# Optimization experiments

Hardware: AMD Instinct MI355X
Metric: run time of the kernel (lower is better)

Reference implementation:

```python
import jax, jax.numpy as jnp
import numpy as np

B, E, DIM, RANK, K, P, H, W, FREQ = 16, 4, 64, 32, 2, 8, 128, 128, 64
NOISE_STD = 1.0 / E


def conv1x1(x, w):
    # x: [b,c,h,w], w: [o,c]
    return jnp.einsum('bchw,oc->bohw', x, w)


def dwconv(x, w, pad):
    # depthwise conv, w: [c,1,kh,kw]
    c = x.shape[1]
    return jax.lax.conv_general_dilated(
        x, w, (1, 1), [(pad, pad), (pad, pad)],
        dimension_numbers=('NCHW', 'OIHW', 'NCHW'), feature_group_count=c)


def patchify(x):
    b, c, h, w = x.shape
    return x.reshape(b, c, h // P, P, w // P, P).transpose(0, 1, 2, 4, 3, 5)


def unpatchify(x):
    b, c, hb, wb, p1, p2 = x.shape
    return x.transpose(0, 1, 2, 4, 3, 5).reshape(b, c, hb * p1, wb * p2)


def chan_layernorm(x, w, b):
    # WithBias LayerNorm over channel dim (to_3d puts c last)
    mu = x.mean(axis=1, keepdims=True)
    var = ((x - mu) ** 2).mean(axis=1, keepdims=True)
    return (x - mu) / jnp.sqrt(var + 1e-5) * w[None, :, None, None] + b[None, :, None, None]


def fft_attention(x, qw, qdw, kvw, kvdw, lnw, lnb, pow_, pob):
    q = dwconv(conv1x1(x, qw), qdw, 1)
    kv = dwconv(conv1x1(x, kvw), kvdw, 3)
    k, v = jnp.split(kv, 2, axis=1)
    qf = jnp.fft.rfft2(patchify(q))
    kf = jnp.fft.rfft2(patchify(k))
    out = jnp.fft.irfft2(qf * kf, s=(P, P))
    out = unpatchify(out)
    out = chan_layernorm(out, lnw, lnb)
    out = out * v
    return conv1x1(out, pow_) + pob[None, :, None, None]


def expert(p0, p1, p2, qw, qdw, kvw, kvdw, lnw, lnb, pow_, pob, x, shared):
    # ModExpert.process (feat_extract with depth>1 recomputes the same value)
    xr = conv1x1(x, p0)
    att = fft_attention(xr, qw, qdw, kvw, kvdw, lnw, lnb, pow_, pob)
    g = jax.nn.silu(conv1x1(shared, p1))
    return conv1x1(att * g, p2) + x


def setup_inputs() -> dict:
    key = jax.random.key(0)
    ks = jax.random.split(key, 20)
    s = 0.05
    return {
        'x': jax.random.normal(ks[0], (B, DIM, H, W), jnp.float32),
        'shared': jax.random.normal(ks[1], (B, DIM, H, W), jnp.float32),
        'freq_emb': jax.random.normal(ks[2], (B, FREQ), jnp.float32),
        'noise': jax.random.normal(ks[3], (B, E), jnp.float32),
        'gate_w': jax.random.normal(ks[4], (E, DIM), jnp.float32) * s,
        'freq_gate_w': jax.random.normal(ks[5], (E, FREQ), jnp.float32) * s,
        'p0': jax.random.normal(ks[6], (E, RANK, DIM), jnp.float32) * s,
        'p1': jax.random.normal(ks[7], (E, RANK, DIM), jnp.float32) * s,
        'p2': jax.random.normal(ks[8], (E, DIM, RANK), jnp.float32) * s,
        'q_w': jax.random.normal(ks[9], (E, RANK, RANK), jnp.float32) * s,
        'q_dw': jax.random.normal(ks[10], (E, RANK, 1, 3, 3), jnp.float32) * s,
        'kv_w': jax.random.normal(ks[11], (E, 2 * RANK, RANK), jnp.float32) * s,
        'kv_dw': jax.random.normal(ks[12], (E, 2 * RANK, 1, 7, 7), jnp.float32) * s,
        'ln_w': jnp.ones((E, RANK), jnp.float32),
        'ln_b': jnp.zeros((E, RANK), jnp.float32),
        'po_w': jax.random.normal(ks[13], (E, RANK, RANK), jnp.float32) * s,
        'po_b': jnp.zeros((E, RANK), jnp.float32),
    }


def reference(x, shared, freq_emb, noise, gate_w, freq_gate_w, p0, p1, p2,
              q_w, q_dw, kv_w, kv_dw, ln_w, ln_b, po_w, po_b):
    # RoutingFunction (eval mode: aux_loss = 0, noise still added)
    pooled = x.mean(axis=(2, 3))                       # [B, DIM]
    logits = pooled @ gate_w.T + freq_emb @ freq_gate_w.T  # [B, E]
    noisy = logits + noise * NOISE_STD
    scores = jax.nn.softmax(noisy, axis=-1)
    vals, idx = jax.lax.top_k(scores, K)
    gates = jnp.zeros_like(scores).at[jnp.arange(B)[:, None], idx].set(vals)
    # Dense expert evaluation; gated combine == SparseDispatcher dispatch/combine
    outs = jax.vmap(expert, in_axes=(0,) * 11 + (None, None))(
        p0, p1, p2, q_w, q_dw, kv_w, kv_dw, ln_w, ln_b, po_w, po_b, x, shared)
    return jnp.einsum('be,ebchw->bchw', gates, outs)
```

## Files before the change

### kernel.cpp

```cpp
#include <hip/hip_runtime.h>
#include <hip/hip_bf16.h>

#define BATCH 16
#define DIM 64
#define RANK 32
#define H 128
#define W 128
#define HW (H*W)
#define NSLOT 32

typedef __attribute__((ext_vector_type(8))) short short8;
typedef __attribute__((ext_vector_type(4))) float f32x4;

static __device__ __forceinline__ float bu2f(unsigned short u) {
    return __uint_as_float(((unsigned)u) << 16);
}
static __device__ __forceinline__ unsigned short f2bu(float f) {
    union { __hip_bfloat16 h; unsigned short u; } cv;
    cv.h = __float2bfloat16(f);
    return cv.u;
}
static __device__ __forceinline__ float ulo(unsigned int w) { return __uint_as_float(w << 16); }
static __device__ __forceinline__ float uhi(unsigned int w) { return __uint_as_float(w & 0xffff0000u); }

__global__ __launch_bounds__(256) void k_pool(const float* __restrict__ x,
                                              float* __restrict__ pooled) {
    int bc = blockIdx.x;
    const float4* p = (const float4*)(x + (size_t)bc * HW);
    float s = 0.f;
    for (int i = threadIdx.x; i < HW / 4; i += 256) {
        float4 v = p[i];
        s += v.x + v.y + v.z + v.w;
    }
#pragma unroll
    for (int off = 32; off > 0; off >>= 1) s += __shfl_down(s, off);
    __shared__ float red[4];
    if ((threadIdx.x & 63) == 0) red[threadIdx.x >> 6] = s;
    __syncthreads();
    if (threadIdx.x == 0)
        pooled[bc] = (red[0] + red[1] + red[2] + red[3]) * (1.f / HW);
}

__global__ __launch_bounds__(64) void k_gate(const float* __restrict__ pooled,
                                             const float* __restrict__ freq_emb,
                                             const float* __restrict__ noise,
                                             const float* __restrict__ gate_w,
                                             const float* __restrict__ fgw,
                                             int* __restrict__ slot_e,
                                             float* __restrict__ slot_g,
                                             float* __restrict__ gsum) {
    int b = threadIdx.x;
    if (b >= BATCH) return;
    float lg[4];
    for (int e = 0; e < 4; e++) {
        float s = 0.f;
        for (int c = 0; c < 64; c++) s += pooled[b * 64 + c] * gate_w[e * 64 + c];
        for (int c = 0; c < 64; c++) s += freq_emb[b * 64 + c] * fgw[e * 64 + c];
        s += noise[b * 4 + e] * 0.25f;
        lg[e] = s;
    }
    float m = fmaxf(fmaxf(lg[0], lg[1]), fmaxf(lg[2], lg[3]));
    float sc[4], Z = 0.f;
    for (int e = 0; e < 4; e++) { sc[e] = expf(lg[e] - m); Z += sc[e]; }
    for (int e = 0; e < 4; e++) sc[e] /= Z;
    int i0 = 0;
    for (int e = 1; e < 4; e++) if (sc[e] > sc[i0]) i0 = e;
    int i1 = -1;
    for (int e = 0; e < 4; e++) {
        if (e == i0) continue;
        if (i1 < 0 || sc[e] > sc[i1]) i1 = e;
    }
    slot_e[2 * b] = i0;     slot_g[2 * b] = sc[i0];
    slot_e[2 * b + 1] = i1; slot_g[2 * b + 1] = sc[i1];
    gsum[b] = sc[i0] + sc[i1];
}

__global__ __launch_bounds__(256) void k_weff(const float* __restrict__ q_w,
                                              const float* __restrict__ kv_w,
                                              const float* __restrict__ p0,
                                              unsigned short* __restrict__ weff_h,
                                              unsigned short* __restrict__ weff_l) {
    int t = blockIdx.x * 256 + threadIdx.x;
    if (t >= 4 * 96 * 64) return;
    int c = t & 63;
    int j = (t >> 6) % 96;
    int e = t / (96 * 64);
    const float* p0p = p0 + (size_t)e * RANK * DIM;
    float s = 0.f;
    if (j < 32) {
        const float* qp = q_w + (e * 32 + j) * 32;
        for (int r = 0; r < 32; r++) s += qp[r] * p0p[r * DIM + c];
    } else {
        const float* kp = kv_w + (e * 64 + (j - 32)) * 32;
        for (int r = 0; r < 32; r++) s += kp[r] * p0p[r * DIM + c];
    }
    int idx = (e * 96 + j) * 64 + c;
    unsigned short hv = f2bu(s);
    weff_h[idx] = hv;
    weff_l[idx] = f2bu(s - bu2f(hv));
}

__global__ __launch_bounds__(256) void k_xpose(const float* __restrict__ po_w,
                                               const float* __restrict__ p1,
                                               float* __restrict__ powf,
                                               float* __restrict__ p1f) {
    int t = blockIdx.x * 256 + threadIdx.x;
    if (t < 4096) {
        int e = t >> 10, oc = (t >> 5) & 31, c = t & 31;
        powf[(e * 32 + c) * 32 + oc] = po_w[t];
    }
    int e = t >> 11, j = (t >> 6) & 31, c = t & 63;
    p1f[(e * 64 + c) * 32 + j] = p1[t];
}

__global__ __launch_bounds__(256) void k_qkvpre(const float* __restrict__ x,
                                                const unsigned short* __restrict__ weff_h,
                                                const unsigned short* __restrict__ weff_l,
                                                const int* __restrict__ slot_e,
                                                unsigned short* __restrict__ qkvpre) {
    __shared__ __align__(16) unsigned short XT[2][128 * 64];
    int blk = blockIdx.x;
    int slot = blk >> 7;
    int p0 = (blk & 127) << 7;
    int b = slot >> 1;
    int e = slot_e[slot];

    {
        int t = threadIdx.x;
        int px = t & 127;
        int ch = (t >> 7) << 5;
        const float* xb = x + ((size_t)b * 64 + ch) * HW + p0 + px;
        unsigned short hv[32] __attribute__((aligned(16)));
        unsigned short lv[32] __attribute__((aligned(16)));
#pragma unroll
        for (int c = 0; c < 32; c++) {
            float v = xb[(size_t)c * HW];
            unsigned short h = f2bu(v);
            hv[c] = h;
            lv[c] = f2bu(v - bu2f(h));
        }
        int rowbyte = px * 128;
        int sw = (px & 7) << 4;
#pragma unroll
        for (int k = 0; k < 4; k++) {
            int byt = (rowbyte + (ch + k * 8) * 2) ^ sw;
            *(uint4*)((char*)XT[0] + byt) = *(const uint4*)&hv[k * 8];
            *(uint4*)((char*)XT[1] + byt) = *(const uint4*)&lv[k * 8];
        }
    }
    __syncthreads();

    int w = threadIdx.x >> 6;
    int l = threadIdx.x & 63;
    int li = l & 15, lq = l >> 4;

    short8 Bf[2][2][2];
#pragma unroll
    for (int nt = 0; nt < 2; nt++) {
        int pxl = (w << 5) + (nt << 4) + li;
        int sw = (pxl & 7) << 4;
#pragma unroll
        for (int kt = 0; kt < 2; kt++) {
            int byt = (pxl * 128 + kt * 64 + lq * 16) ^ sw;
            Bf[nt][kt][0] = *(const short8*)((char*)XT[0] + byt);
            Bf[nt][kt][1] = *(const short8*)((char*)XT[1] + byt);
        }
    }

    const unsigned short* wh = weff_h + ((size_t)e * 96 + li) * 64 + lq * 8;
    const unsigned short* wl = weff_l + ((size_t)e * 96 + li) * 64 + lq * 8;

#pragma unroll
    for (int mt = 0; mt < 6; mt++) {
        short8 Ah[2], Al[2];
#pragma unroll
        for (int kt = 0; kt < 2; kt++) {
            Ah[kt] = *(const short8*)(wh + (mt * 16) * 64 + kt * 32);
            Al[kt] = *(const short8*)(wl + (mt * 16) * 64 + kt * 32);
        }
        f32x4 acc[2] = {{0.f, 0.f, 0.f, 0.f}, {0.f, 0.f, 0.f, 0.f}};
#pragma unroll
        for (int nt = 0; nt < 2; nt++) {
#pragma unroll
            for (int kt = 0; kt < 2; kt++) {
                acc[nt] = __builtin_amdgcn_mfma_f32_16x16x32_bf16(Ah[kt], Bf[nt][kt][0], acc[nt], 0, 0, 0);
                acc[nt] = __builtin_amdgcn_mfma_f32_16x16x32_bf16(Ah[kt], Bf[nt][kt][1], acc[nt], 0, 0, 0);
                acc[nt] = __builtin_amdgcn_mfma_f32_16x16x32_bf16(Al[kt], Bf[nt][kt][0], acc[nt], 0, 0, 0);
            }
        }
#pragma unroll
        for (int nt = 0; nt < 2; nt++) {
            int p = p0 + (w << 5) + (nt << 4) + li;
            unsigned short* op = qkvpre + ((size_t)slot * 96 + mt * 16 + lq * 4) * HW + p;
#pragma unroll
            for (int r = 0; r < 4; r++)
                op[(size_t)r * HW] = f2bu(acc[nt][r]);
        }
    }
}

__global__ __launch_bounds__(256) void k_dw(const unsigned short* __restrict__ qkvpre,
                                            const float* __restrict__ q_dw,
                                            const float* __restrict__ kv_dw,
                                            const int* __restrict__ slot_e,
                                            unsigned short* __restrict__ qkv) {
    __shared__ unsigned short S[38][144];
    int t = blockIdx.x;
    int tile = t & 3;
    int c = (t >> 2) % 96;
    int slot = t / (96 * 4);
    int e = slot_e[slot];
    const unsigned short* in = qkvpre + ((size_t)slot * 96 + c) * HW;
    int y0 = tile * 32 - 3;

    float wk[49];
    if (c < 32) {
        const float* wp = q_dw + (e * 32 + c) * 9;
#pragma unroll
        for (int i = 0; i < 9; i++) wk[i] = wp[i];
    } else {
        const float* wp = kv_dw + (e * 64 + (c - 32)) * 49;
#pragma unroll
        for (int i = 0; i < 49; i++) wk[i] = wp[i];
    }

    for (int i = threadIdx.x; i < 38 * 16; i += 256) {
        int r = i >> 4;
        int xc = (i & 15) << 3;
        int yy = y0 + r;
        uint4 v = make_uint4(0u, 0u, 0u, 0u);
        if (yy >= 0 && yy < H) v = *(const uint4*)(in + (size_t)yy * W + xc);
        *(uint4*)&S[r][8 + xc] = v;
    }
    for (int i = threadIdx.x; i < 38 * 2; i += 256) {
        int r = i >> 1;
        *(uint4*)&S[r][(i & 1) ? 136 : 0] = make_uint4(0u, 0u, 0u, 0u);
    }
    __syncthreads();

    int tx = (threadIdx.x & 31) * 4;
    int ty0 = (threadIdx.x >> 5) * 4;
    float acc[4][4];
#pragma unroll
    for (int a_ = 0; a_ < 4; a_++)
#pragma unroll
        for (int b_ = 0; b_ < 4; b_++) acc[a_][b_] = 0.f;

    if (c < 32) {
#pragma unroll
        for (int rr = 0; rr < 6; rr++) {
            int srow = ty0 + 2 + rr;
            float px[12];
            uint2 w0 = *(const uint2*)&S[srow][4 + tx];
            uint2 w1 = *(const uint2*)&S[srow][8 + tx];
            uint2 w2 = *(const uint2*)&S[srow][12 + tx];
            px[0] = ulo(w0.x); px[1] = uhi(w0.x); px[2] = ulo(w0.y); px[3] = uhi(w0.y);
            px[4] = ulo(w1.x); px[5] = uhi(w1.x); px[6] = ulo(w1.y); px[7] = uhi(w1.y);
            px[8] = ulo(w2.x); px[9] = uhi(w2.x); px[10] = ulo(w2.y); px[11] = uhi(w2.y);
#pragma unroll
            for (int ly = 0; ly < 4; ly++) {
                int ky = rr - ly;
                if (ky < 0 || ky > 2) continue;
#pragma unroll
                for (int kx = 0; kx < 3; kx++) {
                    float wv = wk[ky * 3 + kx];
#pragma unroll
                    for (int j = 0; j < 4; j++) acc[ly][j] += wv * px[j + kx + 3];
                }
            }
        }
    } else {
#pragma unroll
        for (int rr = 0; rr < 10; rr++) {
            int srow = ty0 + rr;
            float px[12];
            uint2 w0 = *(const uint2*)&S[srow][4 + tx];
            uint2 w1 = *(const uint2*)&S[srow][8 + tx];
            uint2 w2 = *(const uint2*)&S[srow][12 + tx];
            px[0] = ulo(w0.x); px[1] = uhi(w0.x); px[2] = ulo(w0.y); px[3] = uhi(w0.y);
            px[4] = ulo(w1.x); px[5] = uhi(w1.x); px[6] = ulo(w1.y); px[7] = uhi(w1.y);
            px[8] = ulo(w2.x); px[9] = uhi(w2.x); px[10] = ulo(w2.y); px[11] = uhi(w2.y);
#pragma unroll
            for (int ly = 0; ly < 4; ly++) {
                int ky = rr - ly;
                if (ky < 0 || ky > 6) continue;
#pragma unroll
                for (int kx = 0; kx < 7; kx++) {
                    float wv = wk[ky * 7 + kx];
#pragma unroll
                    for (int j = 0; j < 4; j++) acc[ly][j] += wv * px[j + kx + 1];
                }
            }
        }
    }

    unsigned short* op = qkv + ((size_t)slot * 96 + c) * HW;
    int ybase = tile * 32 + ty0;
#pragma unroll
    for (int ly = 0; ly < 4; ly++) {
        ushort4 o4;
        o4.x = f2bu(acc[ly][0]); o4.y = f2bu(acc[ly][1]);
        o4.z = f2bu(acc[ly][2]); o4.w = f2bu(acc[ly][3]);
        *(ushort4*)(op + (size_t)(ybase + ly) * W + tx) = o4;
    }
}

__global__ __launch_bounds__(256) void k_circ(const unsigned short* __restrict__ qkv,
                                              unsigned short* __restrict__ obuf) {
    __shared__ float Qs[32][68];
    __shared__ float Kp[32][68];
    int u = threadIdx.x >> 3;
    int i = threadIdx.x & 7;
    int U = blockIdx.x * 32 + u;
    int patch = U & 255;
    int c = (U >> 8) & 31;
    int slot = U >> 13;
    int py = patch >> 4, px = patch & 15;
    size_t rowbase = ((size_t)slot * 96 + c) * HW + (py * 8 + i) * W + px * 8;
    uint4 qu = *(const uint4*)(qkv + rowbase);
    uint4 ku = *(const uint4*)(qkv + rowbase + (size_t)32 * HW);
    float qr[8], kr[8];
    qr[0] = ulo(qu.x); qr[1] = uhi(qu.x); qr[2] = ulo(qu.y); qr[3] = uhi(qu.y);
    qr[4] = ulo(qu.z); qr[5] = uhi(qu.z); qr[6] = ulo(qu.w); qr[7] = uhi(qu.w);
    kr[0] = ulo(ku.x); kr[1] = uhi(ku.x); kr[2] = ulo(ku.y); kr[3] = uhi(ku.y);
    kr[4] = ulo(ku.z); kr[5] = uhi(ku.z); kr[6] = ulo(ku.w); kr[7] = uhi(ku.w);
    *(float4*)&Qs[u][i * 8] = *(float4*)&qr[0];
    *(float4*)&Qs[u][i * 8 + 4] = *(float4*)&qr[4];
    *(float4*)&Kp[u][i * 8] = *(float4*)&kr[0];
    *(float4*)&Kp[u][i * 8 + 4] = *(float4*)&kr[4];
    __syncthreads();
    float acc[8];
#pragma unroll
    for (int j = 0; j < 8; j++) acc[j] = 0.f;
#pragma unroll
    for (int mi = 0; mi < 8; mi++) {
        int r = (i - mi) & 7;
        float qv[8], ka[4], kb[4];
        *(float4*)&qv[0] = *(const float4*)&Qs[u][mi * 8];
        *(float4*)&qv[4] = *(const float4*)&Qs[u][mi * 8 + 4];
        *(float4*)&ka[0] = *(const float4*)&Kp[u][r * 8];
        *(float4*)&kb[0] = *(const float4*)&Kp[u][r * 8 + 4];
#pragma unroll
        for (int j = 0; j < 8; j++) {
            float s = acc[j];
#pragma unroll
            for (int t = 0; t < 4; t++) {
                s += ka[t] * qv[(j - t) & 7];
                s += kb[t] * qv[(j - 4 - t) & 7];
            }
            acc[j] = s;
        }
    }
    size_t obase = ((size_t)slot * 32 + c) * HW + (py * 8 + i) * W + px * 8;
    uint4 ov;
    ov.x = (unsigned)f2bu(acc[0]) | ((unsigned)f2bu(acc[1]) << 16);
    ov.y = (unsigned)f2bu(acc[2]) | ((unsigned)f2bu(acc[3]) << 16);
    ov.z = (unsigned)f2bu(acc[4]) | ((unsigned)f2bu(acc[5]) << 16);
    ov.w = (unsigned)f2bu(acc[6]) | ((unsigned)f2bu(acc[7]) << 16);
    *(uint4*)(obuf + obase) = ov;
}

__global__ __launch_bounds__(256) void k_att(const unsigned short* __restrict__ obuf,
                                             const unsigned short* __restrict__ qkv,
                                             const float* __restrict__ shr,
                                             const int* __restrict__ slot_e,
                                             const float* __restrict__ slot_g,
                                             const float* __restrict__ powf,
                                             const float* __restrict__ po_b,
                                             const float* __restrict__ ln_w,
                                             const float* __restrict__ ln_b,
                                             const float* __restrict__ p1f,
                                             unsigned short* __restrict__ attg) {
    int slot = blockIdx.x >> 6;
    int p = ((blockIdx.x & 63) << 8) + threadIdx.x;
    int b = slot >> 1;
    int e = slot_e[slot];
    float g = slot_g[slot];

    const unsigned short* op = obuf + (size_t)slot * 32 * HW + p;
    float o[32];
#pragma unroll
    for (int c = 0; c < 32; c++) o[c] = bu2f(op[(size_t)c * HW]);
    float mu = 0.f;
#pragma unroll
    for (int c = 0; c < 32; c++) mu += o[c];
    mu *= (1.f / 32.f);
    float var = 0.f;
#pragma unroll
    for (int c = 0; c < 32; c++) { float d = o[c] - mu; var += d * d; }
    float rinv = rsqrtf(var * (1.f / 32.f) + 1e-5f);
    const float* powp = powf + e * 1024;
    const float* lnwp = ln_w + e * 32;
    const float* lnbp = ln_b + e * 32;
    const float* pobp = po_b + e * 32;
    const unsigned short* vp = qkv + ((size_t)slot * 96 + 64) * HW + p;
    float att[32];
#pragma unroll
    for (int j = 0; j < 32; j++) att[j] = pobp[j];
    for (int c = 0; c < 32; c++) {
        float uu = ((o[c] - mu) * rinv * lnwp[c] + lnbp[c]) * bu2f(vp[(size_t)c * HW]);
        const float* pr = powp + c * 32;
#pragma unroll
        for (int j = 0; j < 32; j++) att[j] += pr[j] * uu;
    }

    float t[32];
#pragma unroll
    for (int j = 0; j < 32; j++) t[j] = 0.f;
    const float* shp = shr + (size_t)b * 64 * HW + p;
    const float* p1p = p1f + e * 2048;
    for (int c = 0; c < 64; c++) {
        float sv = shp[(size_t)c * HW];
        const float* pr = p1p + c * 32;
#pragma unroll
        for (int j = 0; j < 32; j++) t[j] += pr[j] * sv;
    }

    unsigned short* ap = attg + ((size_t)slot * HW + p) * 32;
    unsigned int wbuf[16];
#pragma unroll
    for (int jj = 0; jj < 16; jj++) {
        float t0 = t[2 * jj], t1 = t[2 * jj + 1];
        float a0 = g * att[2 * jj] * t0 * __builtin_amdgcn_rcpf(1.f + __expf(-t0));
        float a1 = g * att[2 * jj + 1] * t1 * __builtin_amdgcn_rcpf(1.f + __expf(-t1));
        wbuf[jj] = (unsigned)f2bu(a0) | ((unsigned)f2bu(a1) << 16);
    }
#pragma unroll
    for (int q = 0; q < 4; q++)
        *(uint4*)(ap + q * 8) = *(uint4*)&wbuf[q * 4];
}

__global__ __launch_bounds__(256) void k_comb(const unsigned short* __restrict__ attg,
                                              const float* __restrict__ x,
                                              const int* __restrict__ slot_e,
                                              const float* __restrict__ gsum,
                                              const float* __restrict__ p2,
                                              float* __restrict__ out) {
    int t = blockIdx.x;
    int oh = t & 1;
    int tile = (t >> 1) & 63;
    int b = t >> 7;
    int p = (tile << 8) + threadIdx.x;

    const unsigned short* a0p = attg + ((size_t)(2 * b) * HW + p) * 32;
    const unsigned short* a1p = attg + ((size_t)(2 * b + 1) * HW + p) * 32;
    float a0[32], a1[32];
#pragma unroll
    for (int q = 0; q < 4; q++) {
        uint4 u0 = *(const uint4*)(a0p + q * 8);
        uint4 u1 = *(const uint4*)(a1p + q * 8);
        a0[q * 8 + 0] = ulo(u0.x); a0[q * 8 + 1] = uhi(u0.x);
        a0[q * 8 + 2] = ulo(u0.y); a0[q * 8 + 3] = uhi(u0.y);
        a0[q * 8 + 4] = ulo(u0.z); a0[q * 8 + 5] = uhi(u0.z);
        a0[q * 8 + 6] = ulo(u0.w); a0[q * 8 + 7] = uhi(u0.w);
        a1[q * 8 + 0] = ulo(u1.x); a1[q * 8 + 1] = uhi(u1.x);
        a1[q * 8 + 2] = ulo(u1.y); a1[q * 8 + 3] = uhi(u1.y);
        a1[q * 8 + 4] = ulo(u1.z); a1[q * 8 + 5] = uhi(u1.z);
        a1[q * 8 + 6] = ulo(u1.w); a1[q * 8 + 7] = uhi(u1.w);
    }
    int e0 = slot_e[2 * b], e1 = slot_e[2 * b + 1];
    float gs = gsum[b];
    const float* p2a = p2 + e0 * 2048 + oh * 1024;
    const float* p2b = p2 + e1 * 2048 + oh * 1024;
    const float* xp = x + ((size_t)b * 64 + oh * 32) * HW + p;
    float* oa = out + ((size_t)b * 64 + oh * 32) * HW + p;
    for (int oc = 0; oc < 32; oc++) {
        const float* pa = p2a + oc * 32;
        const float* pb = p2b + oc * 32;
        float sa = 0.f, sb = 0.f;
#pragma unroll
        for (int j = 0; j < 32; j++) {
            sa += pa[j] * a0[j];
            sb += pb[j] * a1[j];
        }
        oa[(size_t)oc * HW] = sa + sb + gs * xp[(size_t)oc * HW];
    }
}

extern "C" void kernel_launch(void* const* d_in, const int* in_sizes, int n_in,
                              void* d_out, int out_size, void* d_ws, size_t ws_size,
                              hipStream_t stream) {
    (void)in_sizes; (void)n_in; (void)out_size; (void)ws_size;
    const float* x      = (const float*)d_in[0];
    const float* shr    = (const float*)d_in[1];
    const float* femb   = (const float*)d_in[2];
    const float* noise  = (const float*)d_in[3];
    const float* gate_w = (const float*)d_in[4];
    const float* fgw    = (const float*)d_in[5];
    const float* p0     = (const float*)d_in[6];
    const float* p1     = (const float*)d_in[7];
    const float* p2     = (const float*)d_in[8];
    const float* q_w    = (const float*)d_in[9];
    const float* q_dw   = (const float*)d_in[10];
    const float* kv_w   = (const float*)d_in[11];
    const float* kv_dw  = (const float*)d_in[12];
    const float* ln_w   = (const float*)d_in[13];
    const float* ln_b   = (const float*)d_in[14];
    const float* po_w   = (const float*)d_in[15];
    const float* po_b   = (const float*)d_in[16];
    float* out = (float*)d_out;

    float* fws = (float*)d_ws;
    float* pooled = fws; fws += 1024;
    float* gsum   = fws; fws += 16;
    float* slot_g = fws; fws += 32;
    int*   slot_e = (int*)fws; fws += 32;
    unsigned short* weffh = (unsigned short*)fws; fws += 12288;
    unsigned short* weffl = (unsigned short*)fws; fws += 12288;
    float* powf   = fws; fws += 4096;
    float* p1f    = fws; fws += 8192;
    uintptr_t a = ((uintptr_t)fws + 255) & ~(uintptr_t)255;
    unsigned short* qkvpre = (unsigned short*)a;
    unsigned short* qkvb   = qkvpre + (size_t)NSLOT * 96 * HW;
    unsigned short* obuf   = qkvb + (size_t)NSLOT * 96 * HW;
    unsigned short* attg   = qkvpre;

    k_pool<<<1024, 256, 0, stream>>>(x, pooled);
    k_gate<<<1, 64, 0, stream>>>(pooled, femb, noise, gate_w, fgw, slot_e, slot_g, gsum);
    k_weff<<<96, 256, 0, stream>>>(q_w, kv_w, p0, weffh, weffl);
    k_xpose<<<32, 256, 0, stream>>>(po_w, p1, powf, p1f);
    k_qkvpre<<<NSLOT * 128, 256, 0, stream>>>(x, weffh, weffl, slot_e, qkvpre);
    k_dw<<<NSLOT * 96 * 4, 256, 0, stream>>>(qkvpre, q_dw, kv_dw, slot_e, qkvb);
    k_circ<<<NSLOT * 32 * 256 / 32, 256, 0, stream>>>(qkvb, obuf);
    k_att<<<NSLOT * 64, 256, 0, stream>>>(obuf, qkvb, shr, slot_e, slot_g,
                                          powf, po_b, ln_w, ln_b, p1f, attg);
    k_comb<<<BATCH * 128, 256, 0, stream>>>(attg, x, slot_e, gsum, p2, out);
}
```

Before: 469.1 us.

## Move attention projection and gate matmuls in k_att onto bf16 MFMA with split precision

k_att used per-thread scalar FMA loops for the 32x32 output projection and the 64->32 gate projection. It now stages the normalized, v-scaled activations and the shared features into LDS as hi/lo bf16 pairs in a swizzled layout. It then computes both projections with 16x16x32 bf16 MFMA instructions, using three products (hi*hi, hi*lo, lo*hi) to keep near-fp32 accuracy. The weight preprocessing kernel now emits hi/lo bf16 copies of po_w and p1 instead of transposed fp32, and the grid doubles to 128 pixels per block. The cost is extra LDS use and conversion work, and half the threads sit idle during each staging branch.

Result: faster. 454.2 us (-3.2%).

```diff
diff --git a/kernel.cpp b/kernel.cpp
--- a/kernel.cpp
+++ b/kernel.cpp
@@ -102,15 +102,21 @@
 
 __global__ __launch_bounds__(256) void k_xpose(const float* __restrict__ po_w,
                                                const float* __restrict__ p1,
-                                               float* __restrict__ powf,
-                                               float* __restrict__ p1f) {
+                                               unsigned short* __restrict__ pow_h,
+                                               unsigned short* __restrict__ pow_l,
+                                               unsigned short* __restrict__ p1_h,
+                                               unsigned short* __restrict__ p1_l) {
     int t = blockIdx.x * 256 + threadIdx.x;
     if (t < 4096) {
-        int e = t >> 10, oc = (t >> 5) & 31, c = t & 31;
-        powf[(e * 32 + c) * 32 + oc] = po_w[t];
-    }
-    int e = t >> 11, j = (t >> 6) & 31, c = t & 63;
-    p1f[(e * 64 + c) * 32 + j] = p1[t];
+        float v = po_w[t];
+        unsigned short h = f2bu(v);
+        pow_h[t] = h;
+        pow_l[t] = f2bu(v - bu2f(h));
+    }
+    float v = p1[t];
+    unsigned short h = f2bu(v);
+    p1_h[t] = h;
+    p1_l[t] = f2bu(v - bu2f(h));
 }
 
 __global__ __launch_bounds__(256) void k_qkvpre(const float* __restrict__ x,
@@ -365,69 +371,155 @@
                                              const float* __restrict__ shr,
                                              const int* __restrict__ slot_e,
                                              const float* __restrict__ slot_g,
-                                             const float* __restrict__ powf,
+                                             const unsigned short* __restrict__ pow_h,
+                                             const unsigned short* __restrict__ pow_l,
                                              const float* __restrict__ po_b,
                                              const float* __restrict__ ln_w,
                                              const float* __restrict__ ln_b,
-                                             const float* __restrict__ p1f,
+                                             const unsigned short* __restrict__ p1_h,
+                                             const unsigned short* __restrict__ p1_l,
                                              unsigned short* __restrict__ attg) {
-    int slot = blockIdx.x >> 6;
-    int p = ((blockIdx.x & 63) << 8) + threadIdx.x;
+    __shared__ __align__(16) unsigned short US[128 * 64];
+    __shared__ __align__(16) unsigned short SS[128 * 128];
+    int blk = blockIdx.x;
+    int slot = blk >> 7;
+    int p0 = (blk & 127) << 7;
     int b = slot >> 1;
     int e = slot_e[slot];
     float g = slot_g[slot];
 
-    const unsigned short* op = obuf + (size_t)slot * 32 * HW + p;
-    float o[32];
-#pragma unroll
-    for (int c = 0; c < 32; c++) o[c] = bu2f(op[(size_t)c * HW]);
-    float mu = 0.f;
-#pragma unroll
-    for (int c = 0; c < 32; c++) mu += o[c];
-    mu *= (1.f / 32.f);
-    float var = 0.f;
-#pragma unroll
-    for (int c = 0; c < 32; c++) { float d = o[c] - mu; var += d * d; }
-    float rinv = rsqrtf(var * (1.f / 32.f) + 1e-5f);
-    const float* powp = powf + e * 1024;
-    const float* lnwp = ln_w + e * 32;
-    const float* lnbp = ln_b + e * 32;
-    const float* pobp = po_b + e * 32;
-    const unsigned short* vp = qkv + ((size_t)slot * 96 + 64) * HW + p;
-    float att[32];
-#pragma unroll
-    for (int j = 0; j < 32; j++) att[j] = pobp[j];
-    for (int c = 0; c < 32; c++) {
-        float uu = ((o[c] - mu) * rinv * lnwp[c] + lnbp[c]) * bu2f(vp[(size_t)c * HW]);
-        const float* pr = powp + c * 32;
-#pragma unroll
-        for (int j = 0; j < 32; j++) att[j] += pr[j] * uu;
-    }
-
-    float t[32];
-#pragma unroll
-    for (int j = 0; j < 32; j++) t[j] = 0.f;
-    const float* shp = shr + (size_t)b * 64 * HW + p;
-    const float* p1p = p1f + e * 2048;
-    for (int c = 0; c < 64; c++) {
-        float sv = shp[(size_t)c * HW];
-        const float* pr = p1p + c * 32;
-#pragma unroll
-        for (int j = 0; j < 32; j++) t[j] += pr[j] * sv;
-    }
-
-    unsigned short* ap = attg + ((size_t)slot * HW + p) * 32;
-    unsigned int wbuf[16];
-#pragma unroll
-    for (int jj = 0; jj < 16; jj++) {
-        float t0 = t[2 * jj], t1 = t[2 * jj + 1];
-        float a0 = g * att[2 * jj] * t0 * __builtin_amdgcn_rcpf(1.f + __expf(-t0));
-        float a1 = g * att[2 * jj + 1] * t1 * __builtin_amdgcn_rcpf(1.f + __expf(-t1));
-        wbuf[jj] = (unsigned)f2bu(a0) | ((unsigned)f2bu(a1) << 16);
-    }
-#pragma unroll
-    for (int q = 0; q < 4; q++)
-        *(uint4*)(ap + q * 8) = *(uint4*)&wbuf[q * 4];
+    {
+        int t = threadIdx.x;
+        int px = t & 127;
+        int sw = (px & 7) << 4;
+        if (t < 128) {
+            const unsigned short* op = obuf + (size_t)slot * 32 * HW + p0 + px;
+            float o[32];
+#pragma unroll
+            for (int c = 0; c < 32; c++) o[c] = bu2f(op[(size_t)c * HW]);
+            float mu = 0.f;
+#pragma unroll
+            for (int c = 0; c < 32; c++) mu += o[c];
+            mu *= (1.f / 32.f);
+            float var = 0.f;
+#pragma unroll
+            for (int c = 0; c < 32; c++) { float d = o[c] - mu; var += d * d; }
+            float rinv = rsqrtf(var * (1.f / 32.f) + 1e-5f);
+            const float* lnwp = ln_w + e * 32;
+            const float* lnbp = ln_b + e * 32;
+            const unsigned short* vp = qkv + ((size_t)slot * 96 + 64) * HW + p0 + px;
+            char* base = (char*)US + px * 128;
+#pragma unroll
+            for (int k = 0; k < 4; k++) {
+                unsigned hq[4], lq_[4];
+#pragma unroll
+                for (int i = 0; i < 4; i++) {
+                    int c0 = k * 8 + i * 2;
+                    float u0 = ((o[c0] - mu) * rinv * lnwp[c0] + lnbp[c0]) * bu2f(vp[(size_t)c0 * HW]);
+                    float u1 = ((o[c0 + 1] - mu) * rinv * lnwp[c0 + 1] + lnbp[c0 + 1]) * bu2f(vp[(size_t)(c0 + 1) * HW]);
+                    unsigned short h0 = f2bu(u0), h1 = f2bu(u1);
+                    hq[i] = (unsigned)h0 | ((unsigned)h1 << 16);
+                    lq_[i] = (unsigned)f2bu(u0 - bu2f(h0)) | ((unsigned)f2bu(u1 - bu2f(h1)) << 16);
+                }
+                *(uint4*)(base + ((k * 16) ^ sw)) = make_uint4(hq[0], hq[1], hq[2], hq[3]);
+                *(uint4*)(base + ((64 + k * 16) ^ sw)) = make_uint4(lq_[0], lq_[1], lq_[2], lq_[3]);
+            }
+        } else {
+            const float* shp = shr + (size_t)b * 64 * HW + p0 + px;
+            char* base = (char*)SS + px * 256;
+#pragma unroll
+            for (int k = 0; k < 8; k++) {
+                unsigned hq[4], lq_[4];
+#pragma unroll
+                for (int i = 0; i < 4; i++) {
+                    int c0 = k * 8 + i * 2;
+                    float v0 = shp[(size_t)c0 * HW];
+                    float v1 = shp[(size_t)(c0 + 1) * HW];
+                    unsigned short h0 = f2bu(v0), h1 = f2bu(v1);
+                    hq[i] = (unsigned)h0 | ((unsigned)h1 << 16);
+                    lq_[i] = (unsigned)f2bu(v0 - bu2f(h0)) | ((unsigned)f2bu(v1 - bu2f(h1)) << 16);
+                }
+                *(uint4*)(base + ((k * 16) ^ sw)) = make_uint4(hq[0], hq[1], hq[2], hq[3]);
+                *(uint4*)(base + 128 + ((k * 16) ^ sw)) = make_uint4(lq_[0], lq_[1], lq_[2], lq_[3]);
+            }
+        }
+    }
+    __syncthreads();
+
+    int w = threadIdx.x >> 6;
+    int l = threadIdx.x & 63;
+    int li = l & 15, lq = l >> 4;
+
+    short8 Bu[2][2];
+    short8 Bs[2][2][2];
+#pragma unroll
+    for (int nt = 0; nt < 2; nt++) {
+        int pxl = (w << 5) + (nt << 4) + li;
+        int sw = (pxl & 7) << 4;
+        char* ub = (char*)US + pxl * 128;
+        Bu[nt][0] = *(const short8*)(ub + ((lq * 16) ^ sw));
+        Bu[nt][1] = *(const short8*)(ub + ((64 + lq * 16) ^ sw));
+        char* sb = (char*)SS + pxl * 256;
+#pragma unroll
+        for (int kt = 0; kt < 2; kt++) {
+            Bs[nt][kt][0] = *(const short8*)(sb + ((kt * 64 + lq * 16) ^ sw));
+            Bs[nt][kt][1] = *(const short8*)(sb + 128 + ((kt * 64 + lq * 16) ^ sw));
+        }
+    }
+
+    f32x4 accA[2][2] = {{{0.f,0.f,0.f,0.f},{0.f,0.f,0.f,0.f}},{{0.f,0.f,0.f,0.f},{0.f,0.f,0.f,0.f}}};
+    f32x4 accT[2][2] = {{{0.f,0.f,0.f,0.f},{0.f,0.f,0.f,0.f}},{{0.f,0.f,0.f,0.f},{0.f,0.f,0.f,0.f}}};
+
+#pragma unroll
+    for (int mt = 0; mt < 2; mt++) {
+        short8 Pah = *(const short8*)(pow_h + ((size_t)e * 32 + mt * 16 + li) * 32 + lq * 8);
+        short8 Pal = *(const short8*)(pow_l + ((size_t)e * 32 + mt * 16 + li) * 32 + lq * 8);
+        short8 Tah[2], Tal[2];
+#pragma unroll
+        for (int kt = 0; kt < 2; kt++) {
+            Tah[kt] = *(const short8*)(p1_h + ((size_t)e * 32 + mt * 16 + li) * 64 + kt * 32 + lq * 8);
+            Tal[kt] = *(const short8*)(p1_l + ((size_t)e * 32 + mt * 16 + li) * 64 + kt * 32 + lq * 8);
+        }
+#pragma unroll
+        for (int nt = 0; nt < 2; nt++) {
+            accA[mt][nt] = __builtin_amdgcn_mfma_f32_16x16x32_bf16(Pah, Bu[nt][0], accA[mt][nt], 0, 0, 0);
+            accA[mt][nt] = __builtin_amdgcn_mfma_f32_16x16x32_bf16(Pah, Bu[nt][1], accA[mt][nt], 0, 0, 0);
+            accA[mt][nt] = __builtin_amdgcn_mfma_f32_16x16x32_bf16(Pal, Bu[nt][0], accA[mt][nt], 0, 0, 0);
+#pragma unroll
+            for (int kt = 0; kt < 2; kt++) {
+                accT[mt][nt] = __builtin_amdgcn_mfma_f32_16x16x32_bf16(Tah[kt], Bs[nt][kt][0], accT[mt][nt], 0, 0, 0);
+                accT[mt][nt] = __builtin_amdgcn_mfma_f32_16x16x32_bf16(Tah[kt], Bs[nt][kt][1], accT[mt][nt], 0, 0, 0);
+                accT[mt][nt] = __builtin_amdgcn_mfma_f32_16x16x32_bf16(Tal[kt], Bs[nt][kt][0], accT[mt][nt], 0, 0, 0);
+            }
+        }
+    }
+
+    float pob[2][4];
+#pragma unroll
+    for (int mt = 0; mt < 2; mt++)
+#pragma unroll
+        for (int r = 0; r < 4; r++)
+            pob[mt][r] = po_b[e * 32 + mt * 16 + lq * 4 + r];
+
+#pragma unroll
+    for (int mt = 0; mt < 2; mt++) {
+#pragma unroll
+        for (int nt = 0; nt < 2; nt++) {
+            unsigned w2[2];
+#pragma unroll
+            for (int rp = 0; rp < 2; rp++) {
+                float attv0 = accA[mt][nt][2 * rp] + pob[mt][2 * rp];
+                float attv1 = accA[mt][nt][2 * rp + 1] + pob[mt][2 * rp + 1];
+                float tv0 = accT[mt][nt][2 * rp];
+                float tv1 = accT[mt][nt][2 * rp + 1];
+                float a0 = g * attv0 * tv0 * __builtin_amdgcn_rcpf(1.f + __expf(-tv0));
+                float a1 = g * attv1 * tv1 * __builtin_amdgcn_rcpf(1.f + __expf(-tv1));
+                w2[rp] = (unsigned)f2bu(a0) | ((unsigned)f2bu(a1) << 16);
+            }
+            int p = p0 + (w << 5) + (nt << 4) + li;
+            *(uint2*)(attg + ((size_t)slot * HW + p) * 32 + mt * 16 + lq * 4) = make_uint2(w2[0], w2[1]);
+        }
+    }
 }
 
 __global__ __launch_bounds__(256) void k_comb(const unsigned short* __restrict__ attg,
@@ -505,10 +597,12 @@
     float* gsum   = fws; fws += 16;
     float* slot_g = fws; fws += 32;
     int*   slot_e = (int*)fws; fws += 32;
-    unsigned short* weffh = (unsigned short*)fws; fws += 12288;
-    unsigned short* weffl = (unsigned short*)fws; fws += 12288;
-    float* powf   = fws; fws += 4096;
-    float* p1f    = fws; fws += 8192;
+    unsigned short* weffh = (unsigned short*)fws; fws += 6144;
+    unsigned short* weffl = (unsigned short*)fws; fws += 6144;
+    unsigned short* pow_h = (unsigned short*)fws; fws += 2048;
+    unsigned short* pow_l = (unsigned short*)fws; fws += 2048;
+    unsigned short* p1a_h = (unsigned short*)fws; fws += 4096;
+    unsigned short* p1a_l = (unsigned short*)fws; fws += 4096;
     uintptr_t a = ((uintptr_t)fws + 255) & ~(uintptr_t)255;
     unsigned short* qkvpre = (unsigned short*)a;
     unsigned short* qkvb   = qkvpre + (size_t)NSLOT * 96 * HW;
@@ -518,11 +612,12 @@
     k_pool<<<1024, 256, 0, stream>>>(x, pooled);
     k_gate<<<1, 64, 0, stream>>>(pooled, femb, noise, gate_w, fgw, slot_e, slot_g, gsum);
     k_weff<<<96, 256, 0, stream>>>(q_w, kv_w, p0, weffh, weffl);
-    k_xpose<<<32, 256, 0, stream>>>(po_w, p1, powf, p1f);
+    k_xpose<<<32, 256, 0, stream>>>(po_w, p1, pow_h, pow_l, p1a_h, p1a_l);
     k_qkvpre<<<NSLOT * 128, 256, 0, stream>>>(x, weffh, weffl, slot_e, qkvpre);
     k_dw<<<NSLOT * 96 * 4, 256, 0, stream>>>(qkvpre, q_dw, kv_dw, slot_e, qkvb);
     k_circ<<<NSLOT * 32 * 256 / 32, 256, 0, stream>>>(qkvb, obuf);
-    k_att<<<NSLOT * 64, 256, 0, stream>>>(obuf, qkvb, shr, slot_e, slot_g,
-                                          powf, po_b, ln_w, ln_b, p1f, attg);
+    k_att<<<NSLOT * 128, 256, 0, stream>>>(obuf, qkvb, shr, slot_e, slot_g,
+                                           pow_h, pow_l, po_b, ln_w, ln_b,
+                                           p1a_h, p1a_l, attg);
     k_comb<<<BATCH * 128, 256, 0, stream>>>(attg, x, slot_e, gsum, p2, out);
 }
```
